# Optimization experiments

Measured on AMD Instinct MI355X. Metric: run time of the kernel, lower is better.

Reference implementation:

```python
import jax, jax.numpy as jnp
import numpy as np

NEGATIVE = 5
MORPH_VOCAB = 200002  # morph_size + 2 (pad + extra row)
D = 128
B = 32768
M = 6


def setup_inputs() -> dict:
    key = jax.random.key(0)
    k = jax.random.split(key, 7)
    data = jax.random.randint(k[0], (B, 2 + 2 * NEGATIVE), 0, 2, dtype=jnp.int64 if jax.config.jax_enable_x64 else jnp.int32)
    word2morph = jax.random.randint(k[1], (B, M), 0, 200000)
    word2morph_mask = jax.random.uniform(k[2], (B, M, 1), dtype=jnp.float32)
    ctx2morph = jax.random.randint(k[3], (B, 1 + NEGATIVE, M), 0, 200000)
    ctx2morph_mask = jax.random.uniform(k[4], (B, 1 + NEGATIVE, M, 1), dtype=jnp.float32)
    # learned tables; torch inits emb0 ~ U(-0.5/D, 0.5/D) and emb1 = 0;
    # use small random values so the reference exercises nontrivial math
    emb0 = jax.random.uniform(k[5], (MORPH_VOCAB, D), minval=-0.5 / D, maxval=0.5 / D, dtype=jnp.float32)
    emb1 = jax.random.uniform(k[6], (MORPH_VOCAB, D), minval=-0.5 / D, maxval=0.5 / D, dtype=jnp.float32)
    return {
        "data": data,
        "word2morph": word2morph,
        "word2morph_mask": word2morph_mask,
        "ctx2morph": ctx2morph,
        "ctx2morph_mask": ctx2morph_mask,
        "emb0": emb0,
        "emb1": emb1,
    }


def reference(data, word2morph, word2morph_mask, ctx2morph, ctx2morph_mask, emb0, emb1):
    neg_mask = data[:, 2 + NEGATIVE:].astype(jnp.float32)              # [B, neg]
    # masked embedding-bag sums over morphemes
    w_embs = jnp.sum(emb0[word2morph] * word2morph_mask, axis=1)        # [B, D]
    c_embs = jnp.sum(emb1[ctx2morph[:, 0]] * ctx2morph_mask[:, 0], axis=1)  # [B, D]
    n_embs = jnp.sum(emb1[ctx2morph[:, 1:1 + NEGATIVE]] * ctx2morph_mask[:, 1:1 + NEGATIVE], axis=2)  # [B, neg, D]
    # dot-product scores
    pos_ips = jnp.sum(w_embs * c_embs, axis=1)                          # [B]
    neg_ips = jnp.einsum("bnd,bd->bn", n_embs, w_embs)                 # [B, neg]
    # clamped logsigmoid losses
    pos_loss = jnp.sum(-jax.nn.log_sigmoid(jnp.clip(pos_ips, -10.0, 10.0)))
    neg_loss = jnp.sum(-jax.nn.log_sigmoid(jnp.clip(-neg_ips, -10.0, 10.0)) * neg_mask)
    return pos_loss + neg_loss
```

## Files before the change

kernel.cpp:

```cpp
#include <hip/hip_runtime.h>

#define NEG 5
#define MM 6
#define NCTX 6
#define DD 128
#define WPB 4
#define RPW 2
#define RPB (WPB * RPW)
#define DROW 12
#define S_SCALE 4096.0f
#define INV_S (1.0f / 4096.0f)

#define SB() __builtin_amdgcn_sched_barrier(0)

typedef float v2f __attribute__((ext_vector_type(2)));

__device__ __forceinline__ int geti(const int4& v, int c) {
    switch (c) { case 0: return v.x; case 1: return v.y; case 2: return v.z; default: return v.w; }
}
__device__ __forceinline__ float getf(const float4& v, int c) {
    switch (c) { case 0: return v.x; case 1: return v.y; case 2: return v.z; default: return v.w; }
}

__global__ __launch_bounds__(256) void cvt_fp8_kernel(
    const float* __restrict__ emb1, unsigned int* __restrict__ q, long n4)
{
    long i = (long)blockIdx.x * 256 + threadIdx.x;
    if (i >= n4) return;
    float4 v = reinterpret_cast<const float4*>(emb1)[i];
    int r = 0;
    r = __builtin_amdgcn_cvt_pk_fp8_f32(v.x * S_SCALE, v.y * S_SCALE, r, false);
    r = __builtin_amdgcn_cvt_pk_fp8_f32(v.z * S_SCALE, v.w * S_SCALE, r, true);
    q[i] = (unsigned int)r;
}

template<int J>
__device__ __forceinline__ void issue_ctx8(unsigned int* dst, const int4& ci, int base,
                                           const unsigned int* __restrict__ q, int sl) {
    #pragma unroll
    for (int m = 0; m < MM; ++m) {
        const int flat = J * MM + m;
        const int k = flat >> 2, c = flat & 3;
        const int idx = __shfl(geti(ci, c), base + k, 64);
        dst[m] = q[(size_t)idx * 32 + sl];
    }
}

template<int J>
__device__ __forceinline__ float consume_dot8(const unsigned int* src, const float4& cmk,
                                              int base, const float4& w) {
    float pj = 0.f;
    #pragma unroll
    for (int m = 0; m < MM; ++m) {
        const int flat = J * MM + m;
        const int k = flat >> 2, c = flat & 3;
        const float mk = __shfl(getf(cmk, c), base + 9 + k, 64);
        v2f lo = __builtin_amdgcn_cvt_pk_f32_fp8(src[m], false);
        v2f hi = __builtin_amdgcn_cvt_pk_f32_fp8(src[m], true);
        pj += mk * (lo[0] * w.x + lo[1] * w.y + hi[0] * w.z + hi[1] * w.w);
    }
    return pj * INV_S;
}

template<int J>
__device__ __forceinline__ void issue_ctx(float4* dst, const int4& ci, int base,
                                          const float* __restrict__ emb1, int d0) {
    #pragma unroll
    for (int m = 0; m < MM; ++m) {
        const int flat = J * MM + m;
        const int k = flat >> 2, c = flat & 3;
        const int idx = __shfl(geti(ci, c), base + k, 64);
        dst[m] = *reinterpret_cast<const float4*>(emb1 + (size_t)idx * DD + d0);
    }
}
template<int J>
__device__ __forceinline__ float consume_dot(const float4* src, const float4& cmk,
                                             int base, const float4& w) {
    float pj = 0.f;
    #pragma unroll
    for (int m = 0; m < MM; ++m) {
        const int flat = J * MM + m;
        const int k = flat >> 2, c = flat & 3;
        const float mk = __shfl(getf(cmk, c), base + 9 + k, 64);
        pj += mk * (src[m].x * w.x + src[m].y * w.y + src[m].z * w.z + src[m].w * w.w);
    }
    return pj;
}

__global__ __launch_bounds__(256) void sg_fused8_kernel(
    const int*   __restrict__ data,
    const int*   __restrict__ w2m,
    const float* __restrict__ w2m_mask,
    const int*   __restrict__ c2m,
    const float* __restrict__ c2m_mask,
    const float* __restrict__ emb0,
    const unsigned int* __restrict__ q,
    float*       __restrict__ out,
    int B)
{
    const int lane  = threadIdx.x & 63;
    const int wid   = threadIdx.x >> 6;
    const int sub   = lane >> 5;
    const int slane = lane & 31;
    const int base  = lane & 32;
    const int b     = blockIdx.x * RPB + wid * RPW + sub;

    float loss = 0.0f;
    if (b < B) {
        int4 ci = {0,0,0,0}; float4 cmk = {0.f,0.f,0.f,0.f};
        int wi = 0; float wmk = 0.f; int nm = 0;
        if (slane < 9)       ci  = reinterpret_cast<const int4*>(c2m + (size_t)b * 36)[slane];
        else if (slane < 18) cmk = reinterpret_cast<const float4*>(c2m_mask + (size_t)b * 36)[slane - 9];
        else if (slane < 24) wi  = w2m[(size_t)b * MM + (slane - 18)];
        else if (slane < 30) wmk = w2m_mask[(size_t)b * MM + (slane - 24)];
        if (slane < NEG) nm = data[(size_t)b * DROW + 2 + NEG + slane];

        float nmf[NEG];
        #pragma unroll
        for (int n = 0; n < NEG; ++n) nmf[n] = (float)__shfl(nm, base + n, 64);

        const int d0 = slane * 4;

        float4 wr[MM];
        #pragma unroll
        for (int m = 0; m < MM; ++m) {
            const int idx = __shfl(wi, base + 18 + m, 64);
            wr[m] = *reinterpret_cast<const float4*>(emb0 + (size_t)idx * DD + d0);
        }
        unsigned int A8[MM], B8[MM], C8[MM], D8[MM], E8[MM], F8[MM];
        issue_ctx8<0>(A8, ci, base, q, slane);
        issue_ctx8<1>(B8, ci, base, q, slane);
        issue_ctx8<2>(C8, ci, base, q, slane);
        issue_ctx8<3>(D8, ci, base, q, slane);
        issue_ctx8<4>(E8, ci, base, q, slane);
        issue_ctx8<5>(F8, ci, base, q, slane);
        SB();

        float4 w = {0.f,0.f,0.f,0.f};
        #pragma unroll
        for (int m = 0; m < MM; ++m) {
            const float mk = __shfl(wmk, base + 24 + m, 64);
            w.x += wr[m].x * mk; w.y += wr[m].y * mk;
            w.z += wr[m].z * mk; w.w += wr[m].w * mk;
        }

        float p[NCTX];
        p[0] = consume_dot8<0>(A8, cmk, base, w);
        p[1] = consume_dot8<1>(B8, cmk, base, w);
        p[2] = consume_dot8<2>(C8, cmk, base, w);
        p[3] = consume_dot8<3>(D8, cmk, base, w);
        p[4] = consume_dot8<4>(E8, cmk, base, w);
        p[5] = consume_dot8<5>(F8, cmk, base, w);

        #pragma unroll
        for (int j = 0; j < NCTX; ++j) {
            float v = p[j];
            #pragma unroll
            for (int off = 16; off >= 1; off >>= 1) v += __shfl_xor(v, off, 64);
            p[j] = v;
        }
        if (slane == 0) {
            float x = fminf(fmaxf(p[0], -10.0f), 10.0f);
            loss = log1pf(expf(-x));
            #pragma unroll
            for (int n = 0; n < NEG; ++n) {
                float y = fminf(fmaxf(-p[1 + n], -10.0f), 10.0f);
                loss += log1pf(expf(-y)) * nmf[n];
            }
        }
    }
    __shared__ float sacc[RPB];
    if (slane == 0) sacc[wid * RPW + sub] = loss;
    __syncthreads();
    if (threadIdx.x == 0) {
        float s = 0.0f;
        #pragma unroll
        for (int i = 0; i < RPB; ++i) s += sacc[i];
        atomicAdd(out, s);
    }
}

__global__ __launch_bounds__(256) void sg_fused_kernel(
    const int*   __restrict__ data,
    const int*   __restrict__ w2m,
    const float* __restrict__ w2m_mask,
    const int*   __restrict__ c2m,
    const float* __restrict__ c2m_mask,
    const float* __restrict__ emb0,
    const float* __restrict__ emb1,
    float*       __restrict__ out,
    int B)
{
    const int lane  = threadIdx.x & 63;
    const int wid   = threadIdx.x >> 6;
    const int sub   = lane >> 5;
    const int slane = lane & 31;
    const int base  = lane & 32;
    const int b     = blockIdx.x * RPB + wid * RPW + sub;

    float loss = 0.0f;
    if (b < B) {
        int4 ci = {0,0,0,0}; float4 cmk = {0.f,0.f,0.f,0.f};
        int wi = 0; float wmk = 0.f; int nm = 0;
        if (slane < 9)       ci  = reinterpret_cast<const int4*>(c2m + (size_t)b * 36)[slane];
        else if (slane < 18) cmk = reinterpret_cast<const float4*>(c2m_mask + (size_t)b * 36)[slane - 9];
        else if (slane < 24) wi  = w2m[(size_t)b * MM + (slane - 18)];
        else if (slane < 30) wmk = w2m_mask[(size_t)b * MM + (slane - 24)];
        if (slane < NEG) nm = data[(size_t)b * DROW + 2 + NEG + slane];

        float nmf[NEG];
        #pragma unroll
        for (int n = 0; n < NEG; ++n) nmf[n] = (float)__shfl(nm, base + n, 64);

        const int d0 = slane * 4;
        float4 wr[MM];
        #pragma unroll
        for (int m = 0; m < MM; ++m) {
            const int idx = __shfl(wi, base + 18 + m, 64);
            wr[m] = *reinterpret_cast<const float4*>(emb0 + (size_t)idx * DD + d0);
        }
        float4 A[MM], Bv[MM], C[MM];
        issue_ctx<0>(A, ci, base, emb1, d0);
        issue_ctx<1>(Bv, ci, base, emb1, d0);
        SB();
        float4 w = {0.f,0.f,0.f,0.f};
        #pragma unroll
        for (int m = 0; m < MM; ++m) {
            const float mk = __shfl(wmk, base + 24 + m, 64);
            w.x += wr[m].x * mk; w.y += wr[m].y * mk;
            w.z += wr[m].z * mk; w.w += wr[m].w * mk;
        }
        issue_ctx<2>(C, ci, base, emb1, d0);
        SB();
        float p[NCTX];
        p[0] = consume_dot<0>(A,  cmk, base, w);  issue_ctx<3>(A,  ci, base, emb1, d0); SB();
        p[1] = consume_dot<1>(Bv, cmk, base, w);  issue_ctx<4>(Bv, ci, base, emb1, d0); SB();
        p[2] = consume_dot<2>(C,  cmk, base, w);  issue_ctx<5>(C,  ci, base, emb1, d0); SB();
        p[3] = consume_dot<3>(A,  cmk, base, w);
        p[4] = consume_dot<4>(Bv, cmk, base, w);
        p[5] = consume_dot<5>(C,  cmk, base, w);

        #pragma unroll
        for (int j = 0; j < NCTX; ++j) {
            float v = p[j];
            #pragma unroll
            for (int off = 16; off >= 1; off >>= 1) v += __shfl_xor(v, off, 64);
            p[j] = v;
        }
        if (slane == 0) {
            float x = fminf(fmaxf(p[0], -10.0f), 10.0f);
            loss = log1pf(expf(-x));
            #pragma unroll
            for (int n = 0; n < NEG; ++n) {
                float y = fminf(fmaxf(-p[1 + n], -10.0f), 10.0f);
                loss += log1pf(expf(-y)) * nmf[n];
            }
        }
    }
    __shared__ float sacc[RPB];
    if (slane == 0) sacc[wid * RPW + sub] = loss;
    __syncthreads();
    if (threadIdx.x == 0) {
        float s = 0.0f;
        #pragma unroll
        for (int i = 0; i < RPB; ++i) s += sacc[i];
        atomicAdd(out, s);
    }
}

extern "C" void kernel_launch(void* const* d_in, const int* in_sizes, int n_in,
                              void* d_out, int out_size, void* d_ws, size_t ws_size,
                              hipStream_t stream) {
    const int*   data     = (const int*)  d_in[0];
    const int*   w2m      = (const int*)  d_in[1];
    const float* w2m_mask = (const float*)d_in[2];
    const int*   c2m      = (const int*)  d_in[3];
    const float* c2m_mask = (const float*)d_in[4];
    const float* emb0     = (const float*)d_in[5];
    const float* emb1     = (const float*)d_in[6];
    float* out = (float*)d_out;

    const int B     = in_sizes[1] / MM;
    const int vocab = in_sizes[6] / DD;
    const int blocks = (B + RPB - 1) / RPB;

    (void)hipMemsetAsync(out, 0, sizeof(float), stream);

    const size_t need = (size_t)vocab * DD;
    if (ws_size >= need) {
        unsigned int* q = (unsigned int*)d_ws;
        const long n4 = (long)vocab * 32;
        const long cvt_blocks = (n4 + 255) / 256;
        cvt_fp8_kernel<<<(int)cvt_blocks, 256, 0, stream>>>(emb1, q, n4);
        sg_fused8_kernel<<<blocks, 64 * WPB, 0, stream>>>(
            data, w2m, w2m_mask, c2m, c2m_mask, emb0, q, out, B);
    } else {
        sg_fused_kernel<<<blocks, 64 * WPB, 0, stream>>>(
            data, w2m, w2m_mask, c2m, c2m_mask, emb0, emb1, out, B);
    }
}
```

Baseline: 97.54 us.

## Move word-embedding bag into fp8 conversion kernel via interleaved blocks

```diff
diff --git a/kernel.cpp b/kernel.cpp
--- a/kernel.cpp
+++ b/kernel.cpp
@@ -22,16 +22,54 @@
     switch (c) { case 0: return v.x; case 1: return v.y; case 2: return v.z; default: return v.w; }
 }
 
-__global__ __launch_bounds__(256) void cvt_fp8_kernel(
-    const float* __restrict__ emb1, unsigned int* __restrict__ q, long n4)
+__global__ __launch_bounds__(256) void sg_prep_kernel(
+    const float* __restrict__ emb1,
+    unsigned int* __restrict__ q,
+    const int*   __restrict__ w2m,
+    const float* __restrict__ w2m_mask,
+    const float* __restrict__ emb0,
+    float*       __restrict__ wbuf,
+    long n4, int B)
 {
-    long i = (long)blockIdx.x * 256 + threadIdx.x;
-    if (i >= n4) return;
-    float4 v = reinterpret_cast<const float4*>(emb1)[i];
-    int r = 0;
-    r = __builtin_amdgcn_cvt_pk_fp8_f32(v.x * S_SCALE, v.y * S_SCALE, r, false);
-    r = __builtin_amdgcn_cvt_pk_fp8_f32(v.z * S_SCALE, v.w * S_SCALE, r, true);
-    q[i] = (unsigned int)r;
+    const int bid = blockIdx.x;
+    if ((bid & 7) == 7) {
+        const int lane  = threadIdx.x & 63;
+        const int wid   = threadIdx.x >> 6;
+        const int sub   = lane >> 5;
+        const int slane = lane & 31;
+        const int base  = lane & 32;
+        const int b     = (bid >> 3) * RPB + wid * RPW + sub;
+        if (b >= B) return;
+
+        int wi = 0; float wmk = 0.f;
+        if (slane < MM)           wi  = w2m[(size_t)b * MM + slane];
+        else if (slane < 2 * MM)  wmk = w2m_mask[(size_t)b * MM + (slane - MM)];
+
+        const int d0 = slane * 4;
+        float4 rr[MM]; float mk[MM];
+        #pragma unroll
+        for (int m = 0; m < MM; ++m) {
+            const int idx = __shfl(wi, base + m, 64);
+            mk[m]         = __shfl(wmk, base + MM + m, 64);
+            rr[m] = *reinterpret_cast<const float4*>(emb0 + (size_t)idx * DD + d0);
+        }
+        float4 acc = {0.f, 0.f, 0.f, 0.f};
+        #pragma unroll
+        for (int m = 0; m < MM; ++m) {
+            acc.x += rr[m].x * mk[m]; acc.y += rr[m].y * mk[m];
+            acc.z += rr[m].z * mk[m]; acc.w += rr[m].w * mk[m];
+        }
+        *reinterpret_cast<float4*>(wbuf + (size_t)b * DD + d0) = acc;
+    } else {
+        const long cvt_id = (long)bid - (bid >> 3);
+        const long i = cvt_id * 256 + threadIdx.x;
+        if (i >= n4) return;
+        float4 v = reinterpret_cast<const float4*>(emb1)[i];
+        int r = 0;
+        r = __builtin_amdgcn_cvt_pk_fp8_f32(v.x * S_SCALE, v.y * S_SCALE, r, false);
+        r = __builtin_amdgcn_cvt_pk_fp8_f32(v.z * S_SCALE, v.w * S_SCALE, r, true);
+        q[i] = (unsigned int)r;
+    }
 }
 
 template<int J>
@@ -62,29 +100,92 @@
     return pj * INV_S;
 }
 
-template<int J>
-__device__ __forceinline__ void issue_ctx(float4* dst, const int4& ci, int base,
-                                          const float* __restrict__ emb1, int d0) {
-    #pragma unroll
-    for (int m = 0; m < MM; ++m) {
-        const int flat = J * MM + m;
-        const int k = flat >> 2, c = flat & 3;
-        const int idx = __shfl(geti(ci, c), base + k, 64);
-        dst[m] = *reinterpret_cast<const float4*>(emb1 + (size_t)idx * DD + d0);
-    }
-}
-template<int J>
-__device__ __forceinline__ float consume_dot(const float4* src, const float4& cmk,
-                                             int base, const float4& w) {
-    float pj = 0.f;
-    #pragma unroll
-    for (int m = 0; m < MM; ++m) {
-        const int flat = J * MM + m;
-        const int k = flat >> 2, c = flat & 3;
-        const float mk = __shfl(getf(cmk, c), base + 9 + k, 64);
-        pj += mk * (src[m].x * w.x + src[m].y * w.y + src[m].z * w.z + src[m].w * w.w);
-    }
-    return pj;
+__global__ __launch_bounds__(256) void sg_dot8_kernel(
+    const int*   __restrict__ data,
+    const int*   __restrict__ c2m,
+    const float* __restrict__ c2m_mask,
+    const unsigned int* __restrict__ q,
+    const float* __restrict__ wbuf,
+    float*       __restrict__ out,
+    int B)
+{
+    const int lane  = threadIdx.x & 63;
+    const int wid   = threadIdx.x >> 6;
+    const int sub   = lane >> 5;
+    const int slane = lane & 31;
+    const int base  = lane & 32;
+    const int b     = blockIdx.x * RPB + wid * RPW + sub;
+
+    float loss = 0.0f;
+    if (b < B) {
+        int4 ci = {0,0,0,0}; float4 cmk = {0.f,0.f,0.f,0.f};
+        int nm = 0;
+        if (slane < 9)       ci  = reinterpret_cast<const int4*>(c2m + (size_t)b * 36)[slane];
+        else if (slane < 18) cmk = reinterpret_cast<const float4*>(c2m_mask + (size_t)b * 36)[slane - 9];
+        if (slane < NEG)     nm  = data[(size_t)b * DROW + 2 + NEG + slane];
+
+        float nmf[NEG];
+        #pragma unroll
+        for (int n = 0; n < NEG; ++n) nmf[n] = (float)__shfl(nm, base + n, 64);
+
+        const int d0 = slane * 4;
+        const float4 w = *reinterpret_cast<const float4*>(wbuf + (size_t)b * DD + d0);
+
+        unsigned int A8[MM], B8[MM], C8[MM], D8[MM], E8[MM], F8[MM];
+        issue_ctx8<0>(A8, ci, base, q, slane);
+        issue_ctx8<1>(B8, ci, base, q, slane);
+        issue_ctx8<2>(C8, ci, base, q, slane);
+        issue_ctx8<3>(D8, ci, base, q, slane);
+        issue_ctx8<4>(E8, ci, base, q, slane);
+        issue_ctx8<5>(F8, ci, base, q, slane);
+        SB();
+
+        float p[NCTX];
+        p[0] = consume_dot8<0>(A8, cmk, base, w);
+        p[1] = consume_dot8<1>(B8, cmk, base, w);
+        p[2] = consume_dot8<2>(C8, cmk, base, w);
+        p[3] = consume_dot8<3>(D8, cmk, base, w);
+        p[4] = consume_dot8<4>(E8, cmk, base, w);
+        p[5] = consume_dot8<5>(F8, cmk, base, w);
+
+        #pragma unroll
+        for (int j = 0; j < NCTX; ++j) {
+            float v = p[j];
+            #pragma unroll
+            for (int off = 16; off >= 1; off >>= 1) v += __shfl_xor(v, off, 64);
+            p[j] = v;
+        }
+        if (slane == 0) {
+            float x = fminf(fmaxf(p[0], -10.0f), 10.0f);
+            loss = log1pf(expf(-x));
+            #pragma unroll
+            for (int n = 0; n < NEG; ++n) {
+                float y = fminf(fmaxf(-p[1 + n], -10.0f), 10.0f);
+                loss += log1pf(expf(-y)) * nmf[n];
+            }
+        }
+    }
+    __shared__ float sacc[RPB];
+    if (slane == 0) sacc[wid * RPW + sub] = loss;
+    __syncthreads();
+    if (threadIdx.x == 0) {
+        float s = 0.0f;
+        #pragma unroll
+        for (int i = 0; i < RPB; ++i) s += sacc[i];
+        atomicAdd(out, s);
+    }
+}
+
+__global__ __launch_bounds__(256) void cvt_fp8_kernel(
+    const float* __restrict__ emb1, unsigned int* __restrict__ q, long n4)
+{
+    long i = (long)blockIdx.x * 256 + threadIdx.x;
+    if (i >= n4) return;
+    float4 v = reinterpret_cast<const float4*>(emb1)[i];
+    int r = 0;
+    r = __builtin_amdgcn_cvt_pk_fp8_f32(v.x * S_SCALE, v.y * S_SCALE, r, false);
+    r = __builtin_amdgcn_cvt_pk_fp8_f32(v.z * S_SCALE, v.w * S_SCALE, r, true);
+    q[i] = (unsigned int)r;
 }
 
 __global__ __launch_bounds__(256) void sg_fused8_kernel(
@@ -120,7 +221,6 @@
         for (int n = 0; n < NEG; ++n) nmf[n] = (float)__shfl(nm, base + n, 64);
 
         const int d0 = slane * 4;
-
         float4 wr[MM];
         #pragma unroll
         for (int m = 0; m < MM; ++m) {
@@ -151,94 +251,6 @@
         p[3] = consume_dot8<3>(D8, cmk, base, w);
         p[4] = consume_dot8<4>(E8, cmk, base, w);
         p[5] = consume_dot8<5>(F8, cmk, base, w);
-
-        #pragma unroll
-        for (int j = 0; j < NCTX; ++j) {
-            float v = p[j];
-            #pragma unroll
-            for (int off = 16; off >= 1; off >>= 1) v += __shfl_xor(v, off, 64);
-            p[j] = v;
-        }
-        if (slane == 0) {
-            float x = fminf(fmaxf(p[0], -10.0f), 10.0f);
-            loss = log1pf(expf(-x));
-            #pragma unroll
-            for (int n = 0; n < NEG; ++n) {
-                float y = fminf(fmaxf(-p[1 + n], -10.0f), 10.0f);
-                loss += log1pf(expf(-y)) * nmf[n];
-            }
-        }
-    }
-    __shared__ float sacc[RPB];
-    if (slane == 0) sacc[wid * RPW + sub] = loss;
-    __syncthreads();
-    if (threadIdx.x == 0) {
-        float s = 0.0f;
-        #pragma unroll
-        for (int i = 0; i < RPB; ++i) s += sacc[i];
-        atomicAdd(out, s);
-    }
-}
-
-__global__ __launch_bounds__(256) void sg_fused_kernel(
-    const int*   __restrict__ data,
-    const int*   __restrict__ w2m,
-    const float* __restrict__ w2m_mask,
-    const int*   __restrict__ c2m,
-    const float* __restrict__ c2m_mask,
-    const float* __restrict__ emb0,
-    const float* __restrict__ emb1,
-    float*       __restrict__ out,
-    int B)
-{
-    const int lane  = threadIdx.x & 63;
-    const int wid   = threadIdx.x >> 6;
-    const int sub   = lane >> 5;
-    const int slane = lane & 31;
-    const int base  = lane & 32;
-    const int b     = blockIdx.x * RPB + wid * RPW + sub;
-
-    float loss = 0.0f;
-    if (b < B) {
-        int4 ci = {0,0,0,0}; float4 cmk = {0.f,0.f,0.f,0.f};
-        int wi = 0; float wmk = 0.f; int nm = 0;
-        if (slane < 9)       ci  = reinterpret_cast<const int4*>(c2m + (size_t)b * 36)[slane];
-        else if (slane < 18) cmk = reinterpret_cast<const float4*>(c2m_mask + (size_t)b * 36)[slane - 9];
-        else if (slane < 24) wi  = w2m[(size_t)b * MM + (slane - 18)];
-        else if (slane < 30) wmk = w2m_mask[(size_t)b * MM + (slane - 24)];
-        if (slane < NEG) nm = data[(size_t)b * DROW + 2 + NEG + slane];
-
-        float nmf[NEG];
-        #pragma unroll
-        for (int n = 0; n < NEG; ++n) nmf[n] = (float)__shfl(nm, base + n, 64);
-
-        const int d0 = slane * 4;
-        float4 wr[MM];
-        #pragma unroll
-        for (int m = 0; m < MM; ++m) {
-            const int idx = __shfl(wi, base + 18 + m, 64);
-            wr[m] = *reinterpret_cast<const float4*>(emb0 + (size_t)idx * DD + d0);
-        }
-        float4 A[MM], Bv[MM], C[MM];
-        issue_ctx<0>(A, ci, base, emb1, d0);
-        issue_ctx<1>(Bv, ci, base, emb1, d0);
-        SB();
-        float4 w = {0.f,0.f,0.f,0.f};
-        #pragma unroll
-        for (int m = 0; m < MM; ++m) {
-            const float mk = __shfl(wmk, base + 24 + m, 64);
-            w.x += wr[m].x * mk; w.y += wr[m].y * mk;
-            w.z += wr[m].z * mk; w.w += wr[m].w * mk;
-        }
-        issue_ctx<2>(C, ci, base, emb1, d0);
-        SB();
-        float p[NCTX];
-        p[0] = consume_dot<0>(A,  cmk, base, w);  issue_ctx<3>(A,  ci, base, emb1, d0); SB();
-        p[1] = consume_dot<1>(Bv, cmk, base, w);  issue_ctx<4>(Bv, ci, base, emb1, d0); SB();
-        p[2] = consume_dot<2>(C,  cmk, base, w);  issue_ctx<5>(C,  ci, base, emb1, d0); SB();
-        p[3] = consume_dot<3>(A,  cmk, base, w);
-        p[4] = consume_dot<4>(Bv, cmk, base, w);
-        p[5] = consume_dot<5>(C,  cmk, base, w);
 
         #pragma unroll
         for (int j = 0; j < NCTX; ++j) {
@@ -286,16 +298,25 @@
 
     (void)hipMemsetAsync(out, 0, sizeof(float), stream);
 
-    const size_t need = (size_t)vocab * DD;
-    if (ws_size >= need) {
+    const size_t qbytes = (size_t)vocab * DD;
+    const size_t wbytes = (size_t)B * DD * sizeof(float);
+    const long   n4     = (long)vocab * 32;
+
+    if (ws_size >= qbytes + wbytes) {
         unsigned int* q = (unsigned int*)d_ws;
-        const long n4 = (long)vocab * 32;
+        float* wbuf = (float*)((char*)d_ws + qbytes);
+        const long cvt_blocks = (n4 + 255) / 256;
+        long grid = 8L * blocks;
+        while (grid - grid / 8 < cvt_blocks) grid += 8;
+        sg_prep_kernel<<<(int)grid, 256, 0, stream>>>(
+            emb1, q, w2m, w2m_mask, emb0, wbuf, n4, B);
+        sg_dot8_kernel<<<blocks, 64 * WPB, 0, stream>>>(
+            data, c2m, c2m_mask, q, wbuf, out, B);
+    } else if (ws_size >= qbytes) {
+        unsigned int* q = (unsigned int*)d_ws;
         const long cvt_blocks = (n4 + 255) / 256;
         cvt_fp8_kernel<<<(int)cvt_blocks, 256, 0, stream>>>(emb1, q, n4);
         sg_fused8_kernel<<<blocks, 64 * WPB, 0, stream>>>(
             data, w2m, w2m_mask, c2m, c2m_mask, emb0, q, out, B);
-    } else {
-        sg_fused_kernel<<<blocks, 64 * WPB, 0, stream>>>(
-            data, w2m, w2m_mask, c2m, c2m_mask, emb0, emb1, out, B);
-    }
-}
+    }
+}
```

Result: slower. 167.0 us (+71.2%).
